# Kernel tuning notes

Measured on AMD Instinct MI355X. Metric: run time of the kernel, lower is better.

The kernel has to match this reference:

```python
import jax, jax.numpy as jnp
import numpy as np

B, N, K = 8, 2048, 16          # clouds, points per cloud, knn k
C_IN, C_OUT, H = 64, 128, 64   # channels; H = hidden of pos_nn/attn_nn MLPs


def _init(key, shape, fan_in):
    return jax.random.normal(key, shape, jnp.float32) / np.sqrt(fan_in)


def setup_inputs() -> dict:
    key = jax.random.key(0)
    ks = jax.random.split(key, 20)
    P = B * N
    inp = {
        "x": jax.random.normal(ks[0], (P, C_IN), jnp.float32),
        "pos": jax.random.uniform(ks[1], (P, 3), jnp.float32),
        "batch": jnp.arange(P, dtype=jnp.int64 if jax.config.jax_enable_x64 else jnp.int32) // N,
        # lin_in: in->in, bias
        "Wi": _init(ks[2], (C_IN, C_IN), C_IN), "bi": jnp.zeros((C_IN,), jnp.float32),
        # PointTransformerConv: lin_src/lin_dst/lin are bias-free Linear(in, out)
        "Wsrc": _init(ks[3], (C_IN, C_OUT), C_IN),
        "Wdst": _init(ks[4], (C_IN, C_OUT), C_IN),
        "Wlin": _init(ks[5], (C_IN, C_OUT), C_IN),
        # pos_nn = MLP([3, 64, out], norm=None, plain_last=False): Lin-ReLU-Lin-ReLU
        "Wp1": _init(ks[6], (3, H), 3), "bp1": jnp.zeros((H,), jnp.float32),
        "Wp2": _init(ks[7], (H, C_OUT), H), "bp2": jnp.zeros((C_OUT,), jnp.float32),
        # attn_nn = MLP([out, 64, out], norm=None, plain_last=False)
        "Wa1": _init(ks[8], (C_OUT, H), C_OUT), "ba1": jnp.zeros((H,), jnp.float32),
        "Wa2": _init(ks[9], (H, C_OUT), H), "ba2": jnp.zeros((C_OUT,), jnp.float32),
        # lin_out: out->out, bias
        "Wo": _init(ks[10], (C_OUT, C_OUT), C_OUT), "bo": jnp.zeros((C_OUT,), jnp.float32),
    }
    return inp


def _knn_with_self(pn):
    # pn: [B,N,3] -> neighbor indices [B,N,K+1] = {self} U kNN (excl self),
    # matching knn_graph(loop=False) followed by conv's add_self_loops.
    sq = jnp.sum(pn * pn, -1)                                   # [B,N]
    d2 = sq[:, :, None] + sq[:, None, :] - 2.0 * jnp.einsum("bnd,bmd->bnm", pn, pn)
    d2 = d2 + jnp.eye(N, dtype=pn.dtype) * 1e10                 # exclude self
    _, idx = jax.lax.top_k(-d2, K)                              # [B,N,K]
    self_idx = jnp.broadcast_to(jnp.arange(N)[None, :, None], (B, N, 1))
    return jnp.concatenate([self_idx, idx], axis=-1)            # [B,N,K+1]


def _forward(x, pos, batch, Wi, bi, Wsrc, Wdst, Wlin, Wp1, bp1, Wp2, bp2,
             Wa1, ba1, Wa2, ba2, Wo, bo):
    # batch is structured as B equal-size clouds of N points (see setup_inputs);
    # knn is computed per-cloud, equivalent to knn_graph(pos, k, batch).
    h = jax.nn.relu(x @ Wi + bi).reshape(B, N, C_IN)            # lin_in + relu
    pn = pos.reshape(B, N, 3)
    nbr = _knn_with_self(pn)                                    # [B,N,K+1]

    gather = jax.vmap(lambda t, i: t[i])                        # [N,C],[N,K+1]->[N,K+1,C]

    a_src = h @ Wsrc                                            # [B,N,C_OUT]
    a_dst = h @ Wdst
    v = h @ Wlin

    rel = pn[:, :, None, :] - gather(pn, nbr)                   # pos_i - pos_j [B,N,K+1,3]
    delta = jax.nn.relu(jax.nn.relu(rel @ Wp1 + bp1) @ Wp2 + bp2)   # pos_nn

    alpha = a_dst[:, :, None, :] - gather(a_src, nbr) + delta   # alpha_i - alpha_j + delta
    attn = jax.nn.relu(jax.nn.relu(alpha @ Wa1 + ba1) @ Wa2 + ba2)  # attn_nn
    w = jax.nn.softmax(attn, axis=2)                            # softmax over neighbors

    msg = w * (gather(v, nbr) + delta)                          # [B,N,K+1,C_OUT]
    out = jnp.mean(msg, axis=2)                                 # aggr='mean' (PyG default here)
    out = out.reshape(B * N, C_OUT)
    return jax.nn.relu(out @ Wo + bo)                           # lin_out + relu


def reference(x, pos, batch, Wi, bi, Wsrc, Wdst, Wlin, Wp1, bp1, Wp2, bp2,
              Wa1, ba1, Wa2, ba2, Wo, bo):
    return _forward(x, pos, batch, Wi, bi, Wsrc, Wdst, Wlin, Wp1, bp1, Wp2, bp2,
                    Wa1, ba1, Wa2, ba2, Wo, bo)
```

## Files before the change

### kernel.cpp

```cpp
#include <hip/hip_runtime.h>
#include <hip/hip_fp16.h>

typedef _Float16 h8 __attribute__((ext_vector_type(8)));
typedef _Float16 h4 __attribute__((ext_vector_type(4)));
typedef float fx4 __attribute__((ext_vector_type(4)));

#define NPTS   2048
#define KP1    17
#define PGPT   4
#define EDGES  68
#define ROWS   80
#define MT     5
#define DELTA_OFF 0
#define PH_OFF    20480
#define ATT_OFF   30720
#define SJ_OFF    30720
#define US_OFF    52224
#define NBR_OFF   53248
#define EDGE_SMEM 53568
#define ATT_RB    168

__device__ __forceinline__ int swzA(int row, int bytecol) {
  return (row << 7) + (bytecol ^ ((row & 7) << 4));
}
__device__ __forceinline__ int swzB(int row, int bytecol) {
  return (row << 8) + (bytecol ^ ((row & 7) << 4));
}

#define KNN_NB   2048
#define GH_NB    256
#define WP_NB    32
#define PK_NB    80
#define P1_GRID  (KNN_NB + GH_NB + WP_NB + PK_NB)

__global__ __launch_bounds__(512) void phase1_kernel(
    const float* __restrict__ pos, int* __restrict__ nbr,
    const float* __restrict__ x, const float* __restrict__ Wi, const float* __restrict__ bi,
    float* __restrict__ h,
    const float* __restrict__ Wdst, const float* __restrict__ Wsrc,
    const float* __restrict__ Wlin, const float* __restrict__ Wa1,
    float* __restrict__ Wall,
    const float* __restrict__ Wp2, const float* __restrict__ Wa2,
    const float* __restrict__ Wo,
    _Float16* __restrict__ p2p, _Float16* __restrict__ a1p, _Float16* __restrict__ a2p,
    _Float16* __restrict__ wop, float* __restrict__ rel)
{
  __shared__ __align__(16) char buf[33792];
  const int bid = blockIdx.x;
  const int tid = threadIdx.x;

  if (bid < KNN_NB) {
    float* px  = (float*)buf;
    float* py  = (float*)(buf + 8192);
    float* pz  = (float*)(buf + 16384);
    float* sqs = (float*)(buf + 24576);
    int p0 = bid * 8;
    int base = (p0 >> 11) << 11;
    for (int i = tid; i < NPTS; i += 512) {
      float xx = pos[(size_t)(base + i) * 3 + 0];
      float yy = pos[(size_t)(base + i) * 3 + 1];
      float zz = pos[(size_t)(base + i) * 3 + 2];
      px[i] = xx; py[i] = yy; pz[i] = zz;
      sqs[i] = xx * xx + yy * yy + zz * zz;
    }
    __syncthreads();
    int wid = tid >> 6, lane = tid & 63;
    int pl = (p0 & 2047) + wid;
    int gp = base + pl;
    float pix = px[pl], piy = py[pl], piz = pz[pl];

    unsigned key[8];
#pragma unroll
    for (int i = 0; i < 8; ++i) key[i] = 0xFFFFFFFFu;
#pragma unroll
    for (int t = 0; t < 32; ++t) {
      int j = t * 64 + lane;
      float dot = pix * px[j] + piy * py[j] + piz * pz[j];
      float dp = __builtin_fmaf(-2.f, dot, sqs[j]) + 4.0f;
      unsigned kb = (__float_as_uint(dp) & 0xFFFFFFE0u) | (unsigned)t;
      kb = (j == pl) ? 0xFFFFFFFFu : kb;
#pragma unroll
      for (int i = 0; i < 8; ++i) {
        unsigned lo = min(key[i], kb), hi = max(key[i], kb);
        key[i] = lo; kb = hi;
      }
    }

    double pxd = (double)pix, pyd = (double)piy, pzd = (double)piz;
    double sqi64 = pxd * pxd + pyd * pyd + pzd * pzd;
    unsigned long long kk[8];
#pragma unroll
    for (int i = 0; i < 8; ++i) {
      if (key[i] == 0xFFFFFFFFu) { kk[i] = 0xFFFFFFFFFFFFFFFFull; continue; }
      int t = key[i] & 31;
      int j = t * 64 + lane;
      double xj = (double)px[j], yj = (double)py[j], zj = (double)pz[j];
      double sqj = xj * xj + yj * yj + zj * zj;
      double dot = pxd * xj + pyd * yj + pzd * zj;
      double d2 = sqi64 + sqj - 2.0 * dot;
      d2 = d2 > 0.0 ? d2 : 0.0;
      unsigned long long bits = (unsigned long long)__double_as_longlong(d2);
      kk[i] = (bits & ~0x7FFull) | (unsigned long long)j;
    }
#define CE(a, b) { unsigned long long lo_ = kk[a] < kk[b] ? kk[a] : kk[b]; \
                   unsigned long long hi_ = kk[a] < kk[b] ? kk[b] : kk[a]; \
                   kk[a] = lo_; kk[b] = hi_; }
    CE(0,1) CE(2,3) CE(4,5) CE(6,7)
    CE(0,2) CE(1,3) CE(4,6) CE(5,7)
    CE(1,2) CE(5,6) CE(0,4) CE(3,7)
    CE(1,5) CE(2,6)
    CE(1,4) CE(3,6)
    CE(2,4) CE(3,5)
    CE(3,4)
#undef CE

    if (lane == 0) nbr[gp * KP1] = gp;
    if (lane < 3)  rel[(size_t)gp * KP1 * 3 + lane] = 0.f;
    for (int it = 0; it < 16; ++it) {
      unsigned h32 = (unsigned)(kk[0] >> 32);
      unsigned key2 = (h32 & ~63u) | (unsigned)lane;
      unsigned m2 = key2;
#pragma unroll
      for (int off = 32; off > 0; off >>= 1) {
        unsigned o = __shfl_xor(m2, off);
        m2 = o < m2 ? o : m2;
      }
      bool same = ((key2 ^ m2) >> 6) == 0;
      unsigned long long ball = __ballot(same);
      int wl; unsigned jwin;
      if (__popcll(ball) == 1) {
        wl = (int)(m2 & 63u);
        unsigned lo32 = (unsigned)kk[0];
        unsigned wlo = __shfl(lo32, wl);
        jwin = wlo & 2047u;
      } else {
        unsigned long long mk = same ? kk[0] : 0xFFFFFFFFFFFFFFFFull;
#pragma unroll
        for (int off = 32; off > 0; off >>= 1) {
          unsigned long long o = __shfl_xor(mk, off);
          mk = o < mk ? o : mk;
        }
        jwin = (unsigned)(mk & 2047ull);
        wl = (int)(jwin & 63u);
      }
      if (lane == 0) nbr[gp * KP1 + 1 + it] = base + (int)jwin;
      if (lane < 3) {
        const float* ps = lane == 0 ? px : (lane == 1 ? py : pz);
        float pi = lane == 0 ? pix : (lane == 1 ? piy : piz);
        rel[((size_t)gp * KP1 + 1 + it) * 3 + lane] = pi - ps[(int)jwin];
      }
      bool mine = (lane == wl);
#pragma unroll
      for (int i = 0; i < 7; ++i) kk[i] = mine ? kk[i + 1] : kk[i];
      kk[7] = mine ? 0xFFFFFFFFFFFFFFFFull : kk[7];
    }
  } else if (bid < KNN_NB + GH_NB) {
    float* As = (float*)buf;
    float* Ws = (float*)(buf + 64 * 68 * 4);
    int b = bid - KNN_NB;
    long row0 = (long)b * 64;
    {
      int r = tid >> 3, k8 = (tid & 7) * 8;
      float4 a0 = *(const float4*)(x + (row0 + r) * 64 + k8);
      float4 a1 = *(const float4*)(x + (row0 + r) * 64 + k8 + 4);
      *(float4*)&As[r * 68 + k8] = a0;
      *(float4*)&As[r * 68 + k8 + 4] = a1;
      float4 w0 = *(const float4*)(Wi + r * 64 + k8);
      float4 w1 = *(const float4*)(Wi + r * 64 + k8 + 4);
      *(float4*)&Ws[r * 64 + k8] = w0;
      *(float4*)&Ws[r * 64 + k8 + 4] = w1;
    }
    __syncthreads();
    int tx = tid & 15, ty = tid >> 4;
    float acc[2][4] = {};
#pragma unroll 8
    for (int k = 0; k < 64; ++k) {
      float4 w = *(const float4*)&Ws[k * 64 + tx * 4];
      float a0 = As[(ty * 2 + 0) * 68 + k];
      float a1 = As[(ty * 2 + 1) * 68 + k];
      acc[0][0] += a0 * w.x; acc[0][1] += a0 * w.y; acc[0][2] += a0 * w.z; acc[0][3] += a0 * w.w;
      acc[1][0] += a1 * w.x; acc[1][1] += a1 * w.y; acc[1][2] += a1 * w.z; acc[1][3] += a1 * w.w;
    }
    float b0 = bi[tx * 4 + 0], b1 = bi[tx * 4 + 1], b2 = bi[tx * 4 + 2], b3 = bi[tx * 4 + 3];
#pragma unroll
    for (int i = 0; i < 2; ++i) {
      float4 o;
      o.x = fmaxf(acc[i][0] + b0, 0.f); o.y = fmaxf(acc[i][1] + b1, 0.f);
      o.z = fmaxf(acc[i][2] + b2, 0.f); o.w = fmaxf(acc[i][3] + b3, 0.f);
      *(float4*)(h + (row0 + ty * 2 + i) * 64 + tx * 4) = o;
    }
  } else if (bid < KNN_NB + GH_NB + WP_NB) {
    int gid = (bid - KNN_NB - GH_NB) * 512 + tid;
    int q = gid >> 12, r = (gid >> 6) & 63, c = gid & 63;
    float val;
    if (q < 2) {
      const float* W = q ? Wsrc : Wdst;
      float acc = 0.f;
      for (int k = 0; k < 128; ++k) acc += W[r * 128 + k] * Wa1[k * 64 + c];
      val = acc;
    } else {
      val = Wlin[r * 128 + (q - 2) * 64 + c];
    }
    Wall[r * 256 + q * 64 + c] = val;
  } else {
    int gid = (bid - KNN_NB - GH_NB - WP_NB) * 512 + tid;
    if (gid < 24576) {
      int m = gid >> 13;
      int r = gid & 8191;
      int tl = r >> 9;
      int l  = (r >> 3) & 63;
      int j  = r & 7;
      const float* src; _Float16* dst; int N, kt, nt;
      if (m == 0)      { src = Wp2; dst = p2p; N = 128; kt = tl & 1; nt = tl >> 1; }
      else if (m == 1) { src = Wa1; dst = a1p; N = 64;  kt = tl & 3; nt = tl >> 2; }
      else             { src = Wa2; dst = a2p; N = 128; kt = tl & 1; nt = tl >> 1; }
      int k = kt * 32 + (l >> 4) * 8 + j;
      int n = nt * 16 + (l & 15);
      dst[r] = (_Float16)src[k * N + n];
    } else {
      int r = gid - 24576;
      int tl = r >> 9;
      int l  = (r >> 3) & 63;
      int j  = r & 7;
      int kt = tl & 3, nt = tl >> 2;
      int k = kt * 32 + (l >> 4) * 8 + j;
      int n = nt * 16 + (l & 15);
      wop[r] = (_Float16)Wo[k * 128 + n];
    }
  }
}

template <int KD, bool BIAS, bool RELU>
__global__ __launch_bounds__(256) void gemm_k(
    const float* __restrict__ A, const float* __restrict__ W,
    const float* __restrict__ bias, float* __restrict__ C, int Nfull) {
  __shared__ float As[64][68];
  __shared__ float Ws[64][64];
  int tid = threadIdx.x;
  int tx = tid & 15, ty = tid >> 4;
  long row0 = (long)blockIdx.x * 64;
  int c0 = blockIdx.y * 64;
  float acc[4][4] = {};
  for (int kb = 0; kb < KD; kb += 64) {
    {
      int k4 = (tid & 15) * 4, r = tid >> 4;
#pragma unroll
      for (int rr = 0; rr < 4; ++rr) {
        float4 a = *(const float4*)(A + (row0 + r + rr * 16) * KD + kb + k4);
        As[r + rr * 16][k4 + 0] = a.x; As[r + rr * 16][k4 + 1] = a.y;
        As[r + rr * 16][k4 + 2] = a.z; As[r + rr * 16][k4 + 3] = a.w;
      }
      int c4 = (tid & 15) * 4, kk = tid >> 4;
#pragma unroll
      for (int rr = 0; rr < 4; ++rr) {
        float4 w = *(const float4*)(W + (size_t)(kb + kk + rr * 16) * Nfull + c0 + c4);
        Ws[kk + rr * 16][c4 + 0] = w.x; Ws[kk + rr * 16][c4 + 1] = w.y;
        Ws[kk + rr * 16][c4 + 2] = w.z; Ws[kk + rr * 16][c4 + 3] = w.w;
      }
    }
    __syncthreads();
#pragma unroll 8
    for (int k = 0; k < 64; ++k) {
      float4 w = *(const float4*)&Ws[k][tx * 4];
      float a0 = As[ty * 4 + 0][k], a1 = As[ty * 4 + 1][k];
      float a2 = As[ty * 4 + 2][k], a3 = As[ty * 4 + 3][k];
      acc[0][0] += a0 * w.x; acc[0][1] += a0 * w.y; acc[0][2] += a0 * w.z; acc[0][3] += a0 * w.w;
      acc[1][0] += a1 * w.x; acc[1][1] += a1 * w.y; acc[1][2] += a1 * w.z; acc[1][3] += a1 * w.w;
      acc[2][0] += a2 * w.x; acc[2][1] += a2 * w.y; acc[2][2] += a2 * w.z; acc[2][3] += a2 * w.w;
      acc[3][0] += a3 * w.x; acc[3][1] += a3 * w.y; acc[3][2] += a3 * w.z; acc[3][3] += a3 * w.w;
    }
    __syncthreads();
  }
#pragma unroll
  for (int i = 0; i < 4; ++i) {
    long row = row0 + ty * 4 + i;
    float4 o;
    float b0 = 0, b1 = 0, b2 = 0, b3 = 0;
    if (BIAS) {
      b0 = bias[c0 + tx * 4 + 0]; b1 = bias[c0 + tx * 4 + 1];
      b2 = bias[c0 + tx * 4 + 2]; b3 = bias[c0 + tx * 4 + 3];
    }
    o.x = acc[i][0] + b0; o.y = acc[i][1] + b1; o.z = acc[i][2] + b2; o.w = acc[i][3] + b3;
    if (RELU) { o.x = fmaxf(o.x, 0.f); o.y = fmaxf(o.y, 0.f); o.z = fmaxf(o.z, 0.f); o.w = fmaxf(o.w, 0.f); }
    *(float4*)(C + row * Nfull + c0 + tx * 4) = o;
  }
}

__global__ __launch_bounds__(512, 6) void edge_kernel(
    const int* __restrict__ nbr,
    const float* __restrict__ usv,
    const float* __restrict__ rel,
    const float* __restrict__ Wp1, const float* __restrict__ bp1,
    const float* __restrict__ bp2, const float* __restrict__ ba1, const float* __restrict__ ba2,
    const _Float16* __restrict__ Wp2p, const _Float16* __restrict__ Wa1p, const _Float16* __restrict__ Wa2p,
    const _Float16* __restrict__ Wop, const float* __restrict__ bo,
    float* __restrict__ out)
{
  __shared__ __align__(16) char smem[EDGE_SMEM];
  int* nbr_s = (int*)(smem + NBR_OFF);
  float* u_s = (float*)(smem + US_OFF);
  const int tid = threadIdx.x;
  const int lane = tid & 63;
  const int wid = tid >> 6;
  const int bid = blockIdx.x;
  const int pb = ((bid & 7) << 9) | (bid >> 3);
  const int p0 = pb * PGPT;

  if (tid < ROWS) nbr_s[tid] = (tid < EDGES) ? nbr[p0 * KP1 + tid] : p0;
  if (tid < PGPT * 64) u_s[tid] = usv[(size_t)(p0 + (tid >> 6)) * 256 + (tid & 63)];
  __syncthreads();

  const int pp5 = tid >> 7;
  const int c5 = tid & 127;
  float vreg[KP1];
#pragma unroll
  for (int k = 0; k < KP1; ++k) {
    int jv = __builtin_amdgcn_readfirstlane(nbr_s[pp5 * KP1 + k]);
    vreg[k] = usv[(size_t)jv * 256 + 128 + c5];
  }

  {
    float w1x = Wp1[lane], w1y = Wp1[64 + lane], w1z = Wp1[128 + lane], b1 = bp1[lane];
    const float* relb = rel + (size_t)p0 * (KP1 * 3);
    for (int e = wid; e < ROWS; e += 8) {
      int ec = min(e, EDGES - 1);
      int eb = __builtin_amdgcn_readfirstlane(ec);
      int j = __builtin_amdgcn_readfirstlane(nbr_s[eb]);
      float sv = usv[(size_t)j * 256 + 64 + lane];
      *(_Float16*)(smem + SJ_OFF + swzA(e, lane * 2)) = (_Float16)sv;
      float rx = relb[eb * 3 + 0];
      float ry = relb[eb * 3 + 1];
      float rz = relb[eb * 3 + 2];
      float acc = fmaxf(b1 + rx * w1x + ry * w1y + rz * w1z, 0.f);
      *(_Float16*)(smem + PH_OFF + swzA(e, lane * 2)) = (_Float16)acc;
    }
  }
  __syncthreads();

  const int rl = lane & 15;
  const int kl = lane >> 4;

  {
    int nt = wid;
    h8 b0 = *(const h8*)(Wp2p + ((size_t)(nt * 2 + 0) * 64 + lane) * 8);
    h8 b1 = *(const h8*)(Wp2p + ((size_t)(nt * 2 + 1) * 64 + lane) * 8);
    int col = nt * 16 + rl;
    float bias2 = bp2[col];
    for (int mt = 0; mt < MT; ++mt) {
      int arow = mt * 16 + rl;
      h8 a0 = *(const h8*)(smem + PH_OFF + swzA(arow, kl * 16));
      h8 a1 = *(const h8*)(smem + PH_OFF + swzA(arow, 64 + kl * 16));
      fx4 acc = {0.f, 0.f, 0.f, 0.f};
      acc = __builtin_amdgcn_mfma_f32_16x16x32_f16(a0, b0, acc, 0, 0, 0);
      acc = __builtin_amdgcn_mfma_f32_16x16x32_f16(a1, b1, acc, 0, 0, 0);
#pragma unroll
      for (int jj = 0; jj < 4; ++jj) {
        int orow = mt * 16 + kl * 4 + jj;
        float val = fmaxf(acc[jj] + bias2, 0.f);
        *(_Float16*)(smem + DELTA_OFF + swzB(orow, col * 2)) = (_Float16)val;
      }
    }
  }
  __syncthreads();

  {
    int nt = wid & 3;
    h8 b[4];
#pragma unroll
    for (int kt = 0; kt < 4; ++kt)
      b[kt] = *(const h8*)(Wa1p + ((size_t)(nt * 4 + kt) * 64 + lane) * 8);
    int hcol = nt * 16 + rl;
    float b1v = ba1[hcol];
    for (int mt = (wid >> 2); mt < MT; mt += 2) {
      int arow = mt * 16 + rl;
      fx4 acc = {0.f, 0.f, 0.f, 0.f};
#pragma unroll
      for (int kt = 0; kt < 4; ++kt) {
        h8 a = *(const h8*)(smem + DELTA_OFF + swzB(arow, kt * 64 + kl * 16));
        acc = __builtin_amdgcn_mfma_f32_16x16x32_f16(a, b[kt], acc, 0, 0, 0);
      }
#pragma unroll
      for (int jj = 0; jj < 4; ++jj) {
        int orow = mt * 16 + kl * 4 + jj;
        int oc = min(orow, EDGES - 1);
        int p = (oc * 241) >> 12;
        float uu = u_s[p * 64 + hcol];
        float ss = (float)*(const _Float16*)(smem + SJ_OFF + swzA(orow, hcol * 2));
        float val = fmaxf(acc[jj] + uu - ss + b1v, 0.f);
        *(_Float16*)(smem + PH_OFF + swzA(orow, hcol * 2)) = (_Float16)val;
      }
    }
  }
  __syncthreads();

  {
    int nt = wid;
    h8 b0 = *(const h8*)(Wa2p + ((size_t)(nt * 2 + 0) * 64 + lane) * 8);
    h8 b1 = *(const h8*)(Wa2p + ((size_t)(nt * 2 + 1) * 64 + lane) * 8);
    int col = nt * 16 + rl;
    float b2v = ba2[col];
    char* cbase = smem + ATT_OFF + col * ATT_RB;
    for (int mt = 0; mt < MT; ++mt) {
      int arow = mt * 16 + rl;
      h8 a0 = *(const h8*)(smem + PH_OFF + swzA(arow, kl * 16));
      h8 a1 = *(const h8*)(smem + PH_OFF + swzA(arow, 64 + kl * 16));
      fx4 acc = {0.f, 0.f, 0.f, 0.f};
      acc = __builtin_amdgcn_mfma_f32_16x16x32_f16(a0, b0, acc, 0, 0, 0);
      acc = __builtin_amdgcn_mfma_f32_16x16x32_f16(a1, b1, acc, 0, 0, 0);
#pragma unroll
      for (int jj = 0; jj < 4; ++jj) {
        int orow = mt * 16 + kl * 4 + jj;
        if (orow < EDGES) {
          int pp = (orow * 241) >> 12;
          float val = fmaxf(acc[jj] + b2v, 0.f);
          *(_Float16*)(cbase + (orow + 3 * pp) * 2) = (_Float16)val;
        }
      }
    }
  }
  __syncthreads();

  h8 bw[4];
#pragma unroll
  for (int kt = 0; kt < 4; ++kt)
    bw[kt] = *(const h8*)(Wop + ((size_t)(wid * 4 + kt) * 64 + lane) * 8);

  {
    int r0 = pp5 * KP1;
    const char* abase = smem + ATT_OFF + c5 * ATT_RB + pp5 * 40;
    h4 t0 = *(const h4*)(abase + 0);
    h4 t1 = *(const h4*)(abase + 8);
    h4 t2 = *(const h4*)(abase + 16);
    h4 t3 = *(const h4*)(abase + 24);
    float att[KP1];
#pragma unroll
    for (int q = 0; q < 4; ++q) {
      att[0 + q]  = (float)t0[q];
      att[4 + q]  = (float)t1[q];
      att[8 + q]  = (float)t2[q];
      att[12 + q] = (float)t3[q];
    }
    att[16] = (float)*(const _Float16*)(abase + 32);
    float m8[8];
#pragma unroll
    for (int k = 0; k < 8; ++k) m8[k] = fmaxf(att[k], att[k + 8]);
    float m4a = fmaxf(m8[0], m8[1]), m4b = fmaxf(m8[2], m8[3]);
    float m4c = fmaxf(m8[4], m8[5]), m4d = fmaxf(m8[6], m8[7]);
    float m = fmaxf(fmaxf(fmaxf(m4a, m4b), fmaxf(m4c, m4d)), att[16]);
    float den = 0.f;
#pragma unroll
    for (int k = 0; k < KP1; ++k) { att[k] = __expf(att[k] - m); den += att[k]; }
    float inv = 1.f / (den * 17.f);
    float acc = 0.f;
#pragma unroll
    for (int k = 0; k < KP1; ++k) {
      float dd = (float)*(const _Float16*)(smem + DELTA_OFF + swzB(r0 + k, c5 * 2));
      acc += att[k] * (vreg[k] + dd);
    }
    *(_Float16*)(smem + PH_OFF + swzB(pp5, c5 * 2)) = (_Float16)(acc * inv);
  }
  __syncthreads();

  {
    fx4 acc = {0.f, 0.f, 0.f, 0.f};
#pragma unroll
    for (int kt = 0; kt < 4; ++kt) {
      h8 a = *(const h8*)(smem + PH_OFF + swzB(rl, kt * 64 + kl * 16));
      acc = __builtin_amdgcn_mfma_f32_16x16x32_f16(a, bw[kt], acc, 0, 0, 0);
    }
    if (kl == 0) {
      int col = wid * 16 + rl;
      float bov = bo[col];
#pragma unroll
      for (int jj = 0; jj < 4; ++jj)
        out[(size_t)(p0 + jj) * 128 + col] = fmaxf(acc[jj] + bov, 0.f);
    }
  }
}

extern "C" void kernel_launch(void* const* d_in, const int* in_sizes, int n_in,
                              void* d_out, int out_size, void* d_ws, size_t ws_size,
                              hipStream_t stream) {
  const float* x    = (const float*)d_in[0];
  const float* pos  = (const float*)d_in[1];
  const float* Wi   = (const float*)d_in[3];
  const float* bi   = (const float*)d_in[4];
  const float* Wsrc = (const float*)d_in[5];
  const float* Wdst = (const float*)d_in[6];
  const float* Wlin = (const float*)d_in[7];
  const float* Wp1  = (const float*)d_in[8];
  const float* bp1  = (const float*)d_in[9];
  const float* Wp2  = (const float*)d_in[10];
  const float* bp2  = (const float*)d_in[11];
  const float* Wa1  = (const float*)d_in[12];
  const float* ba1  = (const float*)d_in[13];
  const float* Wa2  = (const float*)d_in[14];
  const float* ba2  = (const float*)d_in[15];
  const float* Wo   = (const float*)d_in[16];
  const float* bo   = (const float*)d_in[17];
  float* out = (float*)d_out;

  char* ws = (char*)d_ws;
  float* h    = (float*)(ws + 0);
  float* usv  = (float*)(ws + 4194304);
  float* Wall = (float*)(ws + 20971520);
  float* rel  = (float*)(ws + 21037056);
  int*   nbr  = (int*)  (ws + 29360128);
  _Float16* p2p = (_Float16*)(ws + 30474240);
  _Float16* a1p = (_Float16*)(ws + 30490624);
  _Float16* a2p = (_Float16*)(ws + 30507008);
  _Float16* wop = (_Float16*)(ws + 30523392);

  phase1_kernel<<<P1_GRID, 512, 0, stream>>>(pos, nbr, x, Wi, bi, h,
                                             Wdst, Wsrc, Wlin, Wa1, Wall,
                                             Wp2, Wa2, Wo, p2p, a1p, a2p, wop, rel);
  gemm_k<64, false, false><<<dim3(256, 4), 256, 0, stream>>>(h, Wall, nullptr, usv, 256);
  edge_kernel<<<4096, 512, 0, stream>>>(nbr, usv, rel, Wp1, bp1, bp2, ba1, ba2,
                                        p2p, a1p, a2p, wop, bo, out);
}
```

Measured before the change: 143.2 us.

## Move kNN into usv GEMM kernel and hoist edge-kernel weight loads

The kNN search moves out of the phase-1 kernel and into a new kernel that also runs the h·Wall GEMM (replacing gemm_k), so the long-running kNN blocks overlap the usv GEMM instead of the small weight-prep work. The GEMM now uses 512-thread blocks with a 2x4 register tile. In the edge kernel, the neighbor index staging through shared memory and its barrier are removed; indices are read straight from global memory, and the MFMA weight fragments and biases are loaded early to hide latency. The trade-offs are more live registers in the edge kernel and a phase-1 kernel that becomes very short.

Result: slower. 148.1 us (+3.4%).

```diff
diff --git a/kernel.cpp b/kernel.cpp
--- a/kernel.cpp
+++ b/kernel.cpp
@@ -16,8 +16,7 @@
 #define ATT_OFF   30720
 #define SJ_OFF    30720
 #define US_OFF    52224
-#define NBR_OFF   53248
-#define EDGE_SMEM 53568
+#define EDGE_SMEM 53248
 #define ATT_RB    168
 
 __device__ __forceinline__ int swzA(int row, int bytecol) {
@@ -27,14 +26,12 @@
   return (row << 8) + (bytecol ^ ((row & 7) << 4));
 }
 
-#define KNN_NB   2048
 #define GH_NB    256
 #define WP_NB    32
 #define PK_NB    80
-#define P1_GRID  (KNN_NB + GH_NB + WP_NB + PK_NB)
+#define P1_GRID  (GH_NB + WP_NB + PK_NB)
 
 __global__ __launch_bounds__(512) void phase1_kernel(
-    const float* __restrict__ pos, int* __restrict__ nbr,
     const float* __restrict__ x, const float* __restrict__ Wi, const float* __restrict__ bi,
     float* __restrict__ h,
     const float* __restrict__ Wdst, const float* __restrict__ Wsrc,
@@ -43,122 +40,16 @@
     const float* __restrict__ Wp2, const float* __restrict__ Wa2,
     const float* __restrict__ Wo,
     _Float16* __restrict__ p2p, _Float16* __restrict__ a1p, _Float16* __restrict__ a2p,
-    _Float16* __restrict__ wop, float* __restrict__ rel)
+    _Float16* __restrict__ wop)
 {
   __shared__ __align__(16) char buf[33792];
   const int bid = blockIdx.x;
   const int tid = threadIdx.x;
 
-  if (bid < KNN_NB) {
-    float* px  = (float*)buf;
-    float* py  = (float*)(buf + 8192);
-    float* pz  = (float*)(buf + 16384);
-    float* sqs = (float*)(buf + 24576);
-    int p0 = bid * 8;
-    int base = (p0 >> 11) << 11;
-    for (int i = tid; i < NPTS; i += 512) {
-      float xx = pos[(size_t)(base + i) * 3 + 0];
-      float yy = pos[(size_t)(base + i) * 3 + 1];
-      float zz = pos[(size_t)(base + i) * 3 + 2];
-      px[i] = xx; py[i] = yy; pz[i] = zz;
-      sqs[i] = xx * xx + yy * yy + zz * zz;
-    }
-    __syncthreads();
-    int wid = tid >> 6, lane = tid & 63;
-    int pl = (p0 & 2047) + wid;
-    int gp = base + pl;
-    float pix = px[pl], piy = py[pl], piz = pz[pl];
-
-    unsigned key[8];
-#pragma unroll
-    for (int i = 0; i < 8; ++i) key[i] = 0xFFFFFFFFu;
-#pragma unroll
-    for (int t = 0; t < 32; ++t) {
-      int j = t * 64 + lane;
-      float dot = pix * px[j] + piy * py[j] + piz * pz[j];
-      float dp = __builtin_fmaf(-2.f, dot, sqs[j]) + 4.0f;
-      unsigned kb = (__float_as_uint(dp) & 0xFFFFFFE0u) | (unsigned)t;
-      kb = (j == pl) ? 0xFFFFFFFFu : kb;
-#pragma unroll
-      for (int i = 0; i < 8; ++i) {
-        unsigned lo = min(key[i], kb), hi = max(key[i], kb);
-        key[i] = lo; kb = hi;
-      }
-    }
-
-    double pxd = (double)pix, pyd = (double)piy, pzd = (double)piz;
-    double sqi64 = pxd * pxd + pyd * pyd + pzd * pzd;
-    unsigned long long kk[8];
-#pragma unroll
-    for (int i = 0; i < 8; ++i) {
-      if (key[i] == 0xFFFFFFFFu) { kk[i] = 0xFFFFFFFFFFFFFFFFull; continue; }
-      int t = key[i] & 31;
-      int j = t * 64 + lane;
-      double xj = (double)px[j], yj = (double)py[j], zj = (double)pz[j];
-      double sqj = xj * xj + yj * yj + zj * zj;
-      double dot = pxd * xj + pyd * yj + pzd * zj;
-      double d2 = sqi64 + sqj - 2.0 * dot;
-      d2 = d2 > 0.0 ? d2 : 0.0;
-      unsigned long long bits = (unsigned long long)__double_as_longlong(d2);
-      kk[i] = (bits & ~0x7FFull) | (unsigned long long)j;
-    }
-#define CE(a, b) { unsigned long long lo_ = kk[a] < kk[b] ? kk[a] : kk[b]; \
-                   unsigned long long hi_ = kk[a] < kk[b] ? kk[b] : kk[a]; \
-                   kk[a] = lo_; kk[b] = hi_; }
-    CE(0,1) CE(2,3) CE(4,5) CE(6,7)
-    CE(0,2) CE(1,3) CE(4,6) CE(5,7)
-    CE(1,2) CE(5,6) CE(0,4) CE(3,7)
-    CE(1,5) CE(2,6)
-    CE(1,4) CE(3,6)
-    CE(2,4) CE(3,5)
-    CE(3,4)
-#undef CE
-
-    if (lane == 0) nbr[gp * KP1] = gp;
-    if (lane < 3)  rel[(size_t)gp * KP1 * 3 + lane] = 0.f;
-    for (int it = 0; it < 16; ++it) {
-      unsigned h32 = (unsigned)(kk[0] >> 32);
-      unsigned key2 = (h32 & ~63u) | (unsigned)lane;
-      unsigned m2 = key2;
-#pragma unroll
-      for (int off = 32; off > 0; off >>= 1) {
-        unsigned o = __shfl_xor(m2, off);
-        m2 = o < m2 ? o : m2;
-      }
-      bool same = ((key2 ^ m2) >> 6) == 0;
-      unsigned long long ball = __ballot(same);
-      int wl; unsigned jwin;
-      if (__popcll(ball) == 1) {
-        wl = (int)(m2 & 63u);
-        unsigned lo32 = (unsigned)kk[0];
-        unsigned wlo = __shfl(lo32, wl);
-        jwin = wlo & 2047u;
-      } else {
-        unsigned long long mk = same ? kk[0] : 0xFFFFFFFFFFFFFFFFull;
-#pragma unroll
-        for (int off = 32; off > 0; off >>= 1) {
-          unsigned long long o = __shfl_xor(mk, off);
-          mk = o < mk ? o : mk;
-        }
-        jwin = (unsigned)(mk & 2047ull);
-        wl = (int)(jwin & 63u);
-      }
-      if (lane == 0) nbr[gp * KP1 + 1 + it] = base + (int)jwin;
-      if (lane < 3) {
-        const float* ps = lane == 0 ? px : (lane == 1 ? py : pz);
-        float pi = lane == 0 ? pix : (lane == 1 ? piy : piz);
-        rel[((size_t)gp * KP1 + 1 + it) * 3 + lane] = pi - ps[(int)jwin];
-      }
-      bool mine = (lane == wl);
-#pragma unroll
-      for (int i = 0; i < 7; ++i) kk[i] = mine ? kk[i + 1] : kk[i];
-      kk[7] = mine ? 0xFFFFFFFFFFFFFFFFull : kk[7];
-    }
-  } else if (bid < KNN_NB + GH_NB) {
+  if (bid < GH_NB) {
     float* As = (float*)buf;
     float* Ws = (float*)(buf + 64 * 68 * 4);
-    int b = bid - KNN_NB;
-    long row0 = (long)b * 64;
+    long row0 = (long)bid * 64;
     {
       int r = tid >> 3, k8 = (tid & 7) * 8;
       float4 a0 = *(const float4*)(x + (row0 + r) * 64 + k8);
@@ -189,8 +80,8 @@
       o.z = fmaxf(acc[i][2] + b2, 0.f); o.w = fmaxf(acc[i][3] + b3, 0.f);
       *(float4*)(h + (row0 + ty * 2 + i) * 64 + tx * 4) = o;
     }
-  } else if (bid < KNN_NB + GH_NB + WP_NB) {
-    int gid = (bid - KNN_NB - GH_NB) * 512 + tid;
+  } else if (bid < GH_NB + WP_NB) {
+    int gid = (bid - GH_NB) * 512 + tid;
     int q = gid >> 12, r = (gid >> 6) & 63, c = gid & 63;
     float val;
     if (q < 2) {
@@ -203,7 +94,7 @@
     }
     Wall[r * 256 + q * 64 + c] = val;
   } else {
-    int gid = (bid - KNN_NB - GH_NB - WP_NB) * 512 + tid;
+    int gid = (bid - GH_NB - WP_NB) * 512 + tid;
     if (gid < 24576) {
       int m = gid >> 13;
       int r = gid & 8191;
@@ -230,59 +121,158 @@
   }
 }
 
-template <int KD, bool BIAS, bool RELU>
-__global__ __launch_bounds__(256) void gemm_k(
-    const float* __restrict__ A, const float* __restrict__ W,
-    const float* __restrict__ bias, float* __restrict__ C, int Nfull) {
-  __shared__ float As[64][68];
-  __shared__ float Ws[64][64];
-  int tid = threadIdx.x;
-  int tx = tid & 15, ty = tid >> 4;
-  long row0 = (long)blockIdx.x * 64;
-  int c0 = blockIdx.y * 64;
-  float acc[4][4] = {};
-  for (int kb = 0; kb < KD; kb += 64) {
+#define KNN_NB 2048
+#define UG_NB  1024
+#define K2_GRID (KNN_NB + UG_NB)
+
+__global__ __launch_bounds__(512) void knn_usv_kernel(
+    const float* __restrict__ pos, int* __restrict__ nbr, float* __restrict__ rel,
+    const float* __restrict__ h, const float* __restrict__ Wall,
+    float* __restrict__ usv)
+{
+  __shared__ __align__(16) char buf[33792];
+  const int bid = blockIdx.x;
+  const int tid = threadIdx.x;
+
+  if (bid < KNN_NB) {
+    float* px  = (float*)buf;
+    float* py  = (float*)(buf + 8192);
+    float* pz  = (float*)(buf + 16384);
+    float* sqs = (float*)(buf + 24576);
+    int p0 = bid * 8;
+    int base = (p0 >> 11) << 11;
+    for (int i = tid; i < NPTS; i += 512) {
+      float xx = pos[(size_t)(base + i) * 3 + 0];
+      float yy = pos[(size_t)(base + i) * 3 + 1];
+      float zz = pos[(size_t)(base + i) * 3 + 2];
+      px[i] = xx; py[i] = yy; pz[i] = zz;
+      sqs[i] = xx * xx + yy * yy + zz * zz;
+    }
+    __syncthreads();
+    int wid = tid >> 6, lane = tid & 63;
+    int pl = (p0 & 2047) + wid;
+    int gp = base + pl;
+    float pix = px[pl], piy = py[pl], piz = pz[pl];
+
+    unsigned key[8];
+#pragma unroll
+    for (int i = 0; i < 8; ++i) key[i] = 0xFFFFFFFFu;
+#pragma unroll
+    for (int t = 0; t < 32; ++t) {
+      int j = t * 64 + lane;
+      float dot = pix * px[j] + piy * py[j] + piz * pz[j];
+      float dp = __builtin_fmaf(-2.f, dot, sqs[j]) + 4.0f;
+      unsigned kb = (__float_as_uint(dp) & 0xFFFFFFE0u) | (unsigned)t;
+      kb = (j == pl) ? 0xFFFFFFFFu : kb;
+#pragma unroll
+      for (int i = 0; i < 8; ++i) {
+        unsigned lo = min(key[i], kb), hi = max(key[i], kb);
+        key[i] = lo; kb = hi;
+      }
+    }
+
+    double pxd = (double)pix, pyd = (double)piy, pzd = (double)piz;
+    double sqi64 = pxd * pxd + pyd * pyd + pzd * pzd;
+    unsigned long long kk[8];
+#pragma unroll
+    for (int i = 0; i < 8; ++i) {
+      if (key[i] == 0xFFFFFFFFu) { kk[i] = 0xFFFFFFFFFFFFFFFFull; continue; }
+      int t = key[i] & 31;
+      int j = t * 64 + lane;
+      double xj = (double)px[j], yj = (double)py[j], zj = (double)pz[j];
+      double sqj = xj * xj + yj * yj + zj * zj;
+      double dot = pxd * xj + pyd * yj + pzd * zj;
+      double d2 = sqi64 + sqj - 2.0 * dot;
+      d2 = d2 > 0.0 ? d2 : 0.0;
+      unsigned long long bits = (unsigned long long)__double_as_longlong(d2);
+      kk[i] = (bits & ~0x7FFull) | (unsigned long long)j;
+    }
+#define CE(a, b) { unsigned long long lo_ = kk[a] < kk[b] ? kk[a] : kk[b]; \
+                   unsigned long long hi_ = kk[a] < kk[b] ? kk[b] : kk[a]; \
+                   kk[a] = lo_; kk[b] = hi_; }
+    CE(0,1) CE(2,3) CE(4,5) CE(6,7)
+    CE(0,2) CE(1,3) CE(4,6) CE(5,7)
+    CE(1,2) CE(5,6) CE(0,4) CE(3,7)
+    CE(1,5) CE(2,6)
+    CE(1,4) CE(3,6)
+    CE(2,4) CE(3,5)
+    CE(3,4)
+#undef CE
+
+    if (lane == 0) nbr[gp * KP1] = gp;
+    if (lane < 3)  rel[(size_t)gp * KP1 * 3 + lane] = 0.f;
+    for (int it = 0; it < 16; ++it) {
+      unsigned h32 = (unsigned)(kk[0] >> 32);
+      unsigned key2 = (h32 & ~63u) | (unsigned)lane;
+      unsigned m2 = key2;
+#pragma unroll
+      for (int off = 32; off > 0; off >>= 1) {
+        unsigned o = __shfl_xor(m2, off);
+        m2 = o < m2 ? o : m2;
+      }
+      bool same = ((key2 ^ m2) >> 6) == 0;
+      unsigned long long ball = __ballot(same);
+      int wl; unsigned jwin;
+      if (__popcll(ball) == 1) {
+        wl = (int)(m2 & 63u);
+        unsigned lo32 = (unsigned)kk[0];
+        unsigned wlo = __shfl(lo32, wl);
+        jwin = wlo & 2047u;
+      } else {
+        unsigned long long mk = same ? kk[0] : 0xFFFFFFFFFFFFFFFFull;
+#pragma unroll
+        for (int off = 32; off > 0; off >>= 1) {
+          unsigned long long o = __shfl_xor(mk, off);
+          mk = o < mk ? o : mk;
+        }
+        jwin = (unsigned)(mk & 2047ull);
+        wl = (int)(jwin & 63u);
+      }
+      if (lane == 0) nbr[gp * KP1 + 1 + it] = base + (int)jwin;
+      if (lane < 3) {
+        const float* ps = lane == 0 ? px : (lane == 1 ? py : pz);
+        float pi = lane == 0 ? pix : (lane == 1 ? piy : piz);
+        rel[((size_t)gp * KP1 + 1 + it) * 3 + lane] = pi - ps[(int)jwin];
+      }
+      bool mine = (lane == wl);
+#pragma unroll
+      for (int i = 0; i < 7; ++i) kk[i] = mine ? kk[i + 1] : kk[i];
+      kk[7] = mine ? 0xFFFFFFFFFFFFFFFFull : kk[7];
+    }
+  } else {
+    float* As = (float*)buf;
+    float* Ws = (float*)(buf + 64 * 68 * 4);
+    int b2 = bid - KNN_NB;
+    long row0 = (long)(b2 >> 2) * 64;
+    int c0 = (b2 & 3) * 64;
     {
-      int k4 = (tid & 15) * 4, r = tid >> 4;
-#pragma unroll
-      for (int rr = 0; rr < 4; ++rr) {
-        float4 a = *(const float4*)(A + (row0 + r + rr * 16) * KD + kb + k4);
-        As[r + rr * 16][k4 + 0] = a.x; As[r + rr * 16][k4 + 1] = a.y;
-        As[r + rr * 16][k4 + 2] = a.z; As[r + rr * 16][k4 + 3] = a.w;
-      }
-      int c4 = (tid & 15) * 4, kk = tid >> 4;
-#pragma unroll
-      for (int rr = 0; rr < 4; ++rr) {
-        float4 w = *(const float4*)(W + (size_t)(kb + kk + rr * 16) * Nfull + c0 + c4);
-        Ws[kk + rr * 16][c4 + 0] = w.x; Ws[kk + rr * 16][c4 + 1] = w.y;
-        Ws[kk + rr * 16][c4 + 2] = w.z; Ws[kk + rr * 16][c4 + 3] = w.w;
-      }
+      int r = tid >> 3, k8 = (tid & 7) * 8;
+      float4 a0 = *(const float4*)(h + (row0 + r) * 64 + k8);
+      float4 a1 = *(const float4*)(h + (row0 + r) * 64 + k8 + 4);
+      *(float4*)&As[r * 68 + k8] = a0;
+      *(float4*)&As[r * 68 + k8 + 4] = a1;
+      float4 w0 = *(const float4*)(Wall + r * 256 + c0 + k8);
+      float4 w1 = *(const float4*)(Wall + r * 256 + c0 + k8 + 4);
+      *(float4*)&Ws[r * 64 + k8] = w0;
+      *(float4*)&Ws[r * 64 + k8 + 4] = w1;
     }
     __syncthreads();
+    int tx = tid & 15, ty = tid >> 4;
+    float acc[2][4] = {};
 #pragma unroll 8
     for (int k = 0; k < 64; ++k) {
-      float4 w = *(const float4*)&Ws[k][tx * 4];
-      float a0 = As[ty * 4 + 0][k], a1 = As[ty * 4 + 1][k];
-      float a2 = As[ty * 4 + 2][k], a3 = As[ty * 4 + 3][k];
+      float4 w = *(const float4*)&Ws[k * 64 + tx * 4];
+      float a0 = As[(ty * 2 + 0) * 68 + k];
+      float a1 = As[(ty * 2 + 1) * 68 + k];
       acc[0][0] += a0 * w.x; acc[0][1] += a0 * w.y; acc[0][2] += a0 * w.z; acc[0][3] += a0 * w.w;
       acc[1][0] += a1 * w.x; acc[1][1] += a1 * w.y; acc[1][2] += a1 * w.z; acc[1][3] += a1 * w.w;
-      acc[2][0] += a2 * w.x; acc[2][1] += a2 * w.y; acc[2][2] += a2 * w.z; acc[2][3] += a2 * w.w;
-      acc[3][0] += a3 * w.x; acc[3][1] += a3 * w.y; acc[3][2] += a3 * w.z; acc[3][3] += a3 * w.w;
-    }
-    __syncthreads();
-  }
-#pragma unroll
-  for (int i = 0; i < 4; ++i) {
-    long row = row0 + ty * 4 + i;
-    float4 o;
-    float b0 = 0, b1 = 0, b2 = 0, b3 = 0;
-    if (BIAS) {
-      b0 = bias[c0 + tx * 4 + 0]; b1 = bias[c0 + tx * 4 + 1];
-      b2 = bias[c0 + tx * 4 + 2]; b3 = bias[c0 + tx * 4 + 3];
-    }
-    o.x = acc[i][0] + b0; o.y = acc[i][1] + b1; o.z = acc[i][2] + b2; o.w = acc[i][3] + b3;
-    if (RELU) { o.x = fmaxf(o.x, 0.f); o.y = fmaxf(o.y, 0.f); o.z = fmaxf(o.z, 0.f); o.w = fmaxf(o.w, 0.f); }
-    *(float4*)(C + row * Nfull + c0 + tx * 4) = o;
+    }
+#pragma unroll
+    for (int i = 0; i < 2; ++i) {
+      float4 o;
+      o.x = acc[i][0]; o.y = acc[i][1]; o.z = acc[i][2]; o.w = acc[i][3];
+      *(float4*)(usv + (row0 + ty * 2 + i) * 256 + c0 + tx * 4) = o;
+    }
   }
 }
 
@@ -297,35 +287,43 @@
     float* __restrict__ out)
 {
   __shared__ __align__(16) char smem[EDGE_SMEM];
-  int* nbr_s = (int*)(smem + NBR_OFF);
   float* u_s = (float*)(smem + US_OFF);
   const int tid = threadIdx.x;
   const int lane = tid & 63;
   const int wid = tid >> 6;
+  const int rl = lane & 15;
+  const int kl = lane >> 4;
   const int bid = blockIdx.x;
   const int pb = ((bid & 7) << 9) | (bid >> 3);
   const int p0 = pb * PGPT;
-
-  if (tid < ROWS) nbr_s[tid] = (tid < EDGES) ? nbr[p0 * KP1 + tid] : p0;
+  const int* __restrict__ nb = nbr + (size_t)p0 * KP1;
+
   if (tid < PGPT * 64) u_s[tid] = usv[(size_t)(p0 + (tid >> 6)) * 256 + (tid & 63)];
-  __syncthreads();
 
   const int pp5 = tid >> 7;
   const int c5 = tid & 127;
   float vreg[KP1];
 #pragma unroll
   for (int k = 0; k < KP1; ++k) {
-    int jv = __builtin_amdgcn_readfirstlane(nbr_s[pp5 * KP1 + k]);
+    int jv = __builtin_amdgcn_readfirstlane(nb[pp5 * KP1 + k]);
     vreg[k] = usv[(size_t)jv * 256 + 128 + c5];
   }
+
+  h8 p2b0 = *(const h8*)(Wp2p + ((size_t)(wid * 2 + 0) * 64 + lane) * 8);
+  h8 p2b1 = *(const h8*)(Wp2p + ((size_t)(wid * 2 + 1) * 64 + lane) * 8);
+  h8 a1b[4];
+#pragma unroll
+  for (int kt = 0; kt < 4; ++kt)
+    a1b[kt] = *(const h8*)(Wa1p + ((size_t)((wid & 3) * 4 + kt) * 64 + lane) * 8);
+  const float bias2 = bp2[wid * 16 + rl];
+  const float b1v = ba1[(wid & 3) * 16 + rl];
 
   {
     float w1x = Wp1[lane], w1y = Wp1[64 + lane], w1z = Wp1[128 + lane], b1 = bp1[lane];
     const float* relb = rel + (size_t)p0 * (KP1 * 3);
     for (int e = wid; e < ROWS; e += 8) {
-      int ec = min(e, EDGES - 1);
-      int eb = __builtin_amdgcn_readfirstlane(ec);
-      int j = __builtin_amdgcn_readfirstlane(nbr_s[eb]);
+      int eb = __builtin_amdgcn_readfirstlane(min(e, EDGES - 1));
+      int j = __builtin_amdgcn_readfirstlane(nb[eb]);
       float sv = usv[(size_t)j * 256 + 64 + lane];
       *(_Float16*)(smem + SJ_OFF + swzA(e, lane * 2)) = (_Float16)sv;
       float rx = relb[eb * 3 + 0];
@@ -337,22 +335,19 @@
   }
   __syncthreads();
 
-  const int rl = lane & 15;
-  const int kl = lane >> 4;
+  h8 a2b0 = *(const h8*)(Wa2p + ((size_t)(wid * 2 + 0) * 64 + lane) * 8);
+  h8 a2b1 = *(const h8*)(Wa2p + ((size_t)(wid * 2 + 1) * 64 + lane) * 8);
+  const float b2v = ba2[wid * 16 + rl];
 
   {
-    int nt = wid;
-    h8 b0 = *(const h8*)(Wp2p + ((size_t)(nt * 2 + 0) * 64 + lane) * 8);
-    h8 b1 = *(const h8*)(Wp2p + ((size_t)(nt * 2 + 1) * 64 + lane) * 8);
-    int col = nt * 16 + rl;
-    float bias2 = bp2[col];
+    int col = wid * 16 + rl;
     for (int mt = 0; mt < MT; ++mt) {
       int arow = mt * 16 + rl;
       h8 a0 = *(const h8*)(smem + PH_OFF + swzA(arow, kl * 16));
       h8 a1 = *(const h8*)(smem + PH_OFF + swzA(arow, 64 + kl * 16));
       fx4 acc = {0.f, 0.f, 0.f, 0.f};
-      acc = __builtin_amdgcn_mfma_f32_16x16x32_f16(a0, b0, acc, 0, 0, 0);
-      acc = __builtin_amdgcn_mfma_f32_16x16x32_f16(a1, b1, acc, 0, 0, 0);
+      acc = __builtin_amdgcn_mfma_f32_16x16x32_f16(a0, p2b0, acc, 0, 0, 0);
+      acc = __builtin_amdgcn_mfma_f32_16x16x32_f16(a1, p2b1, acc, 0, 0, 0);
 #pragma unroll
       for (int jj = 0; jj < 4; ++jj) {
         int orow = mt * 16 + kl * 4 + jj;
@@ -364,20 +359,14 @@
   __syncthreads();
 
   {
-    int nt = wid & 3;
-    h8 b[4];
-#pragma unroll
-    for (int kt = 0; kt < 4; ++kt)
-      b[kt] = *(const h8*)(Wa1p + ((size_t)(nt * 4 + kt) * 64 + lane) * 8);
-    int hcol = nt * 16 + rl;
-    float b1v = ba1[hcol];
+    int hcol = (wid & 3) * 16 + rl;
     for (int mt = (wid >> 2); mt < MT; mt += 2) {
       int arow = mt * 16 + rl;
       fx4 acc = {0.f, 0.f, 0.f, 0.f};
 #pragma unroll
       for (int kt = 0; kt < 4; ++kt) {
         h8 a = *(const h8*)(smem + DELTA_OFF + swzB(arow, kt * 64 + kl * 16));
-        acc = __builtin_amdgcn_mfma_f32_16x16x32_f16(a, b[kt], acc, 0, 0, 0);
+        acc = __builtin_amdgcn_mfma_f32_16x16x32_f16(a, a1b[kt], acc, 0, 0, 0);
       }
 #pragma unroll
       for (int jj = 0; jj < 4; ++jj) {
@@ -394,19 +383,15 @@
   __syncthreads();
 
   {
-    int nt = wid;
-    h8 b0 = *(const h8*)(Wa2p + ((size_t)(nt * 2 + 0) * 64 + lane) * 8);
-    h8 b1 = *(const h8*)(Wa2p + ((size_t)(nt * 2 + 1) * 64 + lane) * 8);
-    int col = nt * 16 + rl;
-    float b2v = ba2[col];
+    int col = wid * 16 + rl;
     char* cbase = smem + ATT_OFF + col * ATT_RB;
     for (int mt = 0; mt < MT; ++mt) {
       int arow = mt * 16 + rl;
       h8 a0 = *(const h8*)(smem + PH_OFF + swzA(arow, kl * 16));
       h8 a1 = *(const h8*)(smem + PH_OFF + swzA(arow, 64 + kl * 16));
       fx4 acc = {0.f, 0.f, 0.f, 0.f};
-      acc = __builtin_amdgcn_mfma_f32_16x16x32_f16(a0, b0, acc, 0, 0, 0);
-      acc = __builtin_amdgcn_mfma_f32_16x16x32_f16(a1, b1, acc, 0, 0, 0);
+      acc = __builtin_amdgcn_mfma_f32_16x16x32_f16(a0, a2b0, acc, 0, 0, 0);
+      acc = __builtin_amdgcn_mfma_f32_16x16x32_f16(a1, a2b1, acc, 0, 0, 0);
 #pragma unroll
       for (int jj = 0; jj < 4; ++jj) {
         int orow = mt * 16 + kl * 4 + jj;
@@ -511,10 +496,9 @@
   _Float16* a2p = (_Float16*)(ws + 30507008);
   _Float16* wop = (_Float16*)(ws + 30523392);
 
-  phase1_kernel<<<P1_GRID, 512, 0, stream>>>(pos, nbr, x, Wi, bi, h,
-                                             Wdst, Wsrc, Wlin, Wa1, Wall,
-                                             Wp2, Wa2, Wo, p2p, a1p, a2p, wop, rel);
-  gemm_k<64, false, false><<<dim3(256, 4), 256, 0, stream>>>(h, Wall, nullptr, usv, 256);
+  phase1_kernel<<<P1_GRID, 512, 0, stream>>>(x, Wi, bi, h, Wdst, Wsrc, Wlin, Wa1, Wall,
+                                             Wp2, Wa2, Wo, p2p, a1p, a2p, wop);
+  knn_usv_kernel<<<K2_GRID, 512, 0, stream>>>(pos, nbr, rel, h, Wall, usv);
   edge_kernel<<<4096, 512, 0, stream>>>(nbr, usv, rel, Wp1, bp1, bp2, ba1, ba2,
                                         p2p, a1p, a2p, wop, bo, out);
 }
```
